# Optimization experiments

Hardware: AMD Instinct MI355X
Metric: run time of the kernel (lower is better)

Reference implementation:

```python
import jax, jax.numpy as jnp
import numpy as np
import math

B, S, D, H = 2, 2048, 1024, 16
DK = D // H


def setup_inputs() -> dict:
    key = jax.random.key(0)
    ks = jax.random.split(key, 12)
    scale = 1.0 / math.sqrt(D)
    inp = {
        "q": jax.random.normal(ks[0], (B, S, D), jnp.float32),
        "k": jax.random.normal(ks[1], (B, S, D), jnp.float32),
        "v": jax.random.normal(ks[2], (B, S, D), jnp.float32),
        # causal mask, broadcast over batch and heads; 0 entries are masked out
        "mask": jnp.tril(jnp.ones((S, S), jnp.int32))[None, None, :, :],
        "wq_w": jax.random.normal(ks[3], (D, D), jnp.float32) * scale,
        "wq_b": jax.random.normal(ks[4], (D,), jnp.float32) * 0.01,
        "wk_w": jax.random.normal(ks[5], (D, D), jnp.float32) * scale,
        "wk_b": jax.random.normal(ks[6], (D,), jnp.float32) * 0.01,
        "wv_w": jax.random.normal(ks[7], (D, D), jnp.float32) * scale,
        "wv_b": jax.random.normal(ks[8], (D,), jnp.float32) * 0.01,
        "wo_w": jax.random.normal(ks[9], (D, D), jnp.float32) * scale,
        "wo_b": jax.random.normal(ks[10], (D,), jnp.float32) * 0.01,
    }
    return inp


def _mha(q, k, v, mask, wq_w, wq_b, wk_w, wk_b, wv_w, wv_b, wo_w, wo_b):
    # nn.Linear: x @ W^T + b
    def split_heads(x):  # [B,S,D] -> [B,H,S,DK]
        return x.reshape(B, S, H, DK).transpose(0, 2, 1, 3)

    Q = split_heads(q @ wq_w.T + wq_b)
    K = split_heads(k @ wk_w.T + wk_b)
    V = split_heads(v @ wv_w.T + wv_b)

    scores = jnp.einsum("bhqd,bhkd->bhqk", Q, K) / math.sqrt(DK)  # [B,H,S,S]
    scores = jnp.where(mask == 0, jnp.float32(-1e9), scores)
    # NOTE: source uses softmax(dim=1) == over the HEADS axis; replicated faithfully.
    attn = jax.nn.softmax(scores, axis=1)
    out = jnp.einsum("bhqk,bhkd->bhqd", attn, V)  # [B,H,S,DK]
    out = out.transpose(0, 2, 1, 3).reshape(B, S, D)
    return out @ wo_w.T + wo_b


def reference(q, k, v, mask, wq_w, wq_b, wk_w, wk_b, wv_w, wv_b, wo_w, wo_b):
    return _mha(q, k, v, mask, wq_w, wq_b, wk_w, wk_b, wv_w, wv_b, wo_w, wo_b)
```

## Files before the change

kernel.cpp:

```cpp
#include <hip/hip_runtime.h>
#include <stdint.h>


#define BB 2
#define SS 2048
#define DD 1024
#define HH 16
#define DKK 64

typedef _Float16 f16;
typedef __attribute__((ext_vector_type(2))) _Float16 f16x2;
typedef __attribute__((ext_vector_type(8))) _Float16 f16x8;
typedef __attribute__((ext_vector_type(2))) __fp16 fp16x2_raw;
typedef __attribute__((ext_vector_type(4))) float f32x4;

typedef __attribute__((address_space(3))) uint32_t lds32_t;
typedef __attribute__((address_space(1))) uint32_t g32_t;

__device__ __forceinline__ void async_cp16(void* lds, const void* g){
    __builtin_amdgcn_global_load_lds((const g32_t*)g, (lds32_t*)lds, 16, 0, 0);
}

union U32H { uint32_t u; f16x2 h; fp16x2_raw hr; };

__device__ __forceinline__ uint32_t pk2(float a, float b){
    U32H c; c.hr = __builtin_amdgcn_cvt_pkrtz(a, b); return c.u;
}
__device__ __forceinline__ float h_lo(uint32_t w){ U32H c; c.u = w; return (float)c.h[0]; }
__device__ __forceinline__ float h_hi(uint32_t w){ U32H c; c.u = w; return (float)c.h[1]; }
__device__ __forceinline__ uint32_t pkmul(uint32_t a, uint32_t b){
    U32H x, y, r; x.u = a; y.u = b; r.h = x.h * y.h; return r.u;
}
__device__ __forceinline__ uint32_t pkadd(uint32_t a, uint32_t b){
    U32H x, y, r; x.u = a; y.u = b; r.h = x.h + y.h; return r.u;
}
__device__ __forceinline__ uint16_t f2h(float f){
    union { f16 h; uint16_t u; } c; c.h = (f16)f; return c.u;
}

__global__ __launch_bounds__(256) void cvt_all(
    const float* __restrict__ w0, const float* __restrict__ w1,
    const float* __restrict__ w2, const float* __restrict__ w3,
    const float* __restrict__ a0, const float* __restrict__ a1,
    const float* __restrict__ a2,
    uint16_t* __restrict__ dw0, uint16_t* __restrict__ dw1,
    uint16_t* __restrict__ dw2, uint16_t* __restrict__ dw3,
    uint16_t* __restrict__ da0, uint16_t* __restrict__ da1,
    uint16_t* __restrict__ da2)
{
    const int y = blockIdx.y;
    const float* s; uint16_t* d; int n4;
    switch (y) {
        case 0: s = w0; d = dw0; n4 = 262144; break;
        case 1: s = w1; d = dw1; n4 = 262144; break;
        case 2: s = w2; d = dw2; n4 = 262144; break;
        case 3: s = w3; d = dw3; n4 = 262144; break;
        case 4: s = a0; d = da0; n4 = 1048576; break;
        case 5: s = a1; d = da1; n4 = 1048576; break;
        default: s = a2; d = da2; n4 = 1048576; break;
    }
    int i = blockIdx.x * 256 + threadIdx.x;
    if (i >= n4) return;
    float4 v = ((const float4*)s)[i];
    ((uint2*)d)[i] = make_uint2(pk2(v.x, v.y), pk2(v.z, v.w));
}

template <int OMODE>
__device__ __forceinline__ void gemm_core(
    uint16_t (*As)[32], uint16_t (*Bs)[32],
    const uint16_t* __restrict__ A, const uint16_t* __restrict__ W,
    const float* __restrict__ bias, void* __restrict__ Cout,
    const int kbeg, const int kend)
{
    const int t    = threadIdx.x;
    const int bm   = blockIdx.x * 128;
    const int bn   = blockIdx.y * 128;
    const int lane = t & 63;
    const int w    = t >> 6;
    const int wm   = (w >> 1) * 64;
    const int wn   = (w & 1) * 64;
    const int lm   = lane & 15;
    const int quad = lane >> 4;

    f32x4 acc[4][4] = {};

    const int lr = lane >> 2;
    const int lc = (lane & 3) * 8;

    for (int k0 = kbeg; k0 < kend; k0 += 32) {
#pragma unroll
        for (int i2 = 0; i2 < 2; ++i2) {
            const int i = w * 2 + i2;
            async_cp16(&As[16*i][0], &A[(size_t)(bm + 16*i + lr) * DD + k0 + lc]);
            async_cp16(&Bs[16*i][0], &W[(size_t)(bn + 16*i + lr) * DD + k0 + lc]);
        }
        __syncthreads();
        f16x8 a8[4], b8[4];
#pragma unroll
        for (int mt = 0; mt < 4; ++mt) a8[mt] = *(const f16x8*)&As[wm + 16*mt + lm][quad*8];
#pragma unroll
        for (int nt = 0; nt < 4; ++nt) b8[nt] = *(const f16x8*)&Bs[wn + 16*nt + lm][quad*8];
#pragma unroll
        for (int mt = 0; mt < 4; ++mt)
#pragma unroll
            for (int nt = 0; nt < 4; ++nt)
                acc[mt][nt] = __builtin_amdgcn_mfma_f32_16x16x32_f16(a8[mt], b8[nt], acc[mt][nt], 0, 0, 0);
        __syncthreads();
    }

#pragma unroll
    for (int nt = 0; nt < 4; ++nt) {
        const int ng = bn + wn + 16*nt + lm;
        const float bv = bias ? bias[ng] : 0.0f;
#pragma unroll
        for (int mt = 0; mt < 4; ++mt) {
            const int m0 = bm + wm + 16*mt + quad*4;
            if (OMODE == 1) {
                const int bb = m0 >> 11, s0 = m0 & (SS - 1);
                const int hh = ng >> 6,  dk = ng & 63;
                uint2 wv;
                wv.x = pk2(acc[mt][nt][0] + bv, acc[mt][nt][1] + bv);
                wv.y = pk2(acc[mt][nt][2] + bv, acc[mt][nt][3] + bv);
                *(uint2*)&((uint16_t*)Cout)[(((size_t)(bb*HH + hh))*DKK + dk)*SS + s0] = wv;
            } else {
#pragma unroll
                for (int r = 0; r < 4; ++r) {
                    const int m = m0 + r;
                    const float val = acc[mt][nt][r] + bv;
                    if (OMODE == 0) {
                        const int bb = m >> 11, s = m & (SS - 1);
                        const int hh = ng >> 6, dk = ng & 63;
                        ((uint16_t*)Cout)[(((size_t)(bb*HH + hh))*SS + s)*DKK + dk] = f2h(val);
                    } else {
                        ((float*)Cout)[(size_t)m * DD + ng] = val;
                    }
                }
            }
        }
    }
}

__global__ __launch_bounds__(256) void gemm_qkv(
    const uint16_t* __restrict__ xq, const uint16_t* __restrict__ wq,
    const float* __restrict__ bq, uint16_t* __restrict__ Qc,
    const uint16_t* __restrict__ xk, const uint16_t* __restrict__ wk,
    const float* __restrict__ bk, uint16_t* __restrict__ Kc,
    const uint16_t* __restrict__ xv, const uint16_t* __restrict__ wv,
    const float* __restrict__ bv, uint16_t* __restrict__ Vt)
{
    __shared__ __align__(16) uint16_t As[128][32];
    __shared__ __align__(16) uint16_t Bs[128][32];
    const int z = blockIdx.z;
    if (z == 0)      gemm_core<0>(As, Bs, xq, wq, bq, Qc, 0, DD);
    else if (z == 1) gemm_core<0>(As, Bs, xk, wk, bk, Kc, 0, DD);
    else             gemm_core<1>(As, Bs, xv, wv, bv, Vt, 0, DD);
}

__global__ __launch_bounds__(256) void gemm_o_split(
    const uint16_t* __restrict__ A, const uint16_t* __restrict__ W,
    const float* __restrict__ bias, float* __restrict__ P0, float* __restrict__ P1)
{
    __shared__ __align__(16) uint16_t As[128][32];
    __shared__ __align__(16) uint16_t Bs[128][32];
    const int z = blockIdx.z;
    if (z == 0) gemm_core<2>(As, Bs, A, W, bias,    (void*)P0, 0,   512);
    else        gemm_core<2>(As, Bs, A, W, nullptr, (void*)P1, 512, 1024);
}

__global__ __launch_bounds__(256) void addf4(
    const float* __restrict__ a, const float* __restrict__ b, float* __restrict__ o)
{
    const int i = blockIdx.x * 256 + threadIdx.x;
    float4 x = ((const float4*)a)[i];
    float4 y = ((const float4*)b)[i];
    ((float4*)o)[i] = make_float4(x.x+y.x, x.y+y.y, x.z+y.z, x.w+y.w);
}

__global__ __launch_bounds__(256) void suf_kernel(
    const uint16_t* __restrict__ Vt, float* __restrict__ Suf)
{
    const int bh = blockIdx.x;
    const int t  = threadIdx.x;
    const int d = t & 63, seg = t >> 6;
    __shared__ float cs[64][65];
    const uint16_t* row = Vt + ((size_t)bh * DKK + d) * SS;
    for (int cl = 0; cl < 16; ++cl) {
        const int c = seg * 16 + cl;
        float sum = 0.f;
#pragma unroll
        for (int jj = 0; jj < 4; ++jj) {
            uint4 u = *(const uint4*)&row[c * 32 + jj * 8];
            sum += ((h_lo(u.x)+h_hi(u.x)) + (h_lo(u.y)+h_hi(u.y)))
                 + ((h_lo(u.z)+h_hi(u.z)) + (h_lo(u.w)+h_hi(u.w)));
        }
        cs[c][d] = sum;
    }
    __syncthreads();
    if (t < 64) {
        float run = 0.f;
        Suf[((size_t)bh * 65 + 64) * DKK + t] = 0.f;
        for (int c = 63; c >= 0; --c) {
            run += cs[c][t];
            Suf[((size_t)bh * 65 + c) * DKK + t] = run;
        }
    }
}

__global__ __launch_bounds__(1024, 4) void attn_v11(
    const uint16_t* __restrict__ Qc, const uint16_t* __restrict__ Kc,
    const uint16_t* __restrict__ Vt, const float* __restrict__ Suf,
    uint16_t* __restrict__ AOp)
{
    __shared__ __align__(16) uint16_t E[3][16][32][40];
    __shared__ __align__(16) uint16_t Zr[2][32][40];

    const int x  = blockIdx.x;
    const int p  = x & 3;
    const int b  = (x >> 2) & 1;
    const int pr = x >> 3;
    const int tid  = threadIdx.x;
    const int h    = tid >> 6;
    const int lane = tid & 63;
    const int lm   = lane & 15;
    const int quad = lane >> 4;

    const uint16_t* Qh = Qc + ((size_t)(b*HH + h)) * SS * DKK;
    const uint16_t* Kh = Kc + ((size_t)(b*HH + h)) * SS * DKK;
    const uint16_t* Vh = Vt + ((size_t)(b*HH + h)) * DKK * SS;
    uint16_t* AOb = AOp + ((size_t)(p*BB + b)) * SS * DD;

    const int rq  = tid >> 4;
    const int rk2 = tid & 15;

#pragma unroll
    for (int tt = 0; tt < 2; ++tt) {
        const int tq = tt ? (63 - pr) : pr;
        const int q0 = tq * 32;
        const int nch = (tq >= p) ? ((tq - p) >> 2) + 1 : 0;

        f16x8 qf[2][2];
#pragma unroll
        for (int qt = 0; qt < 2; ++qt)
#pragma unroll
            for (int kd = 0; kd < 2; ++kd)
                qf[qt][kd] = *(const f16x8*)&Qh[(size_t)(q0 + 16*qt + lm)*DKK + kd*32 + quad*8];

        f32x4 oacc[2][4] = {};

        auto LOADK = [&](int c, f16x8* kf) {
            const int k0 = c * 32;
#pragma unroll
            for (int kt = 0; kt < 2; ++kt) {
                kf[2*kt+0] = *(const f16x8*)&Kh[(size_t)(k0 + 16*kt + lm)*DKK + quad*8];
                kf[2*kt+1] = *(const f16x8*)&Kh[(size_t)(k0 + 16*kt + lm)*DKK + 32 + quad*8];
            }
        };
        auto LOADV = [&](int c, f16x8* vf) {
            const int k0 = c * 32;
#pragma unroll
            for (int dt = 0; dt < 4; ++dt)
                vf[dt] = *(const f16x8*)&Vh[(size_t)(16*dt + lm)*SS + k0 + quad*8];
        };

        auto SCORES_C = [&](int c, int ebw, const f16x8* kf) {
            const int k0 = c * 32;
            f32x4 sacc[2][2] = {};
#pragma unroll
            for (int kt = 0; kt < 2; ++kt)
#pragma unroll
                for (int qt = 0; qt < 2; ++qt) {
                    sacc[kt][qt] = __builtin_amdgcn_mfma_f32_16x16x32_f16(kf[2*kt+0], qf[qt][0], sacc[kt][qt], 0, 0, 0);
                    sacc[kt][qt] = __builtin_amdgcn_mfma_f32_16x16x32_f16(kf[2*kt+1], qf[qt][1], sacc[kt][qt], 0, 0, 0);
                }
#pragma unroll
            for (int kt = 0; kt < 2; ++kt)
#pragma unroll
                for (int qt = 0; qt < 2; ++qt) {
                    const int kh = k0 + 16*kt, qh = q0 + 16*qt;
                    uint2 evw;
                    if (kh + 15 <= qh) {
                        evw.x = pk2(__expf(sacc[kt][qt][0] * 0.125f), __expf(sacc[kt][qt][1] * 0.125f));
                        evw.y = pk2(__expf(sacc[kt][qt][2] * 0.125f), __expf(sacc[kt][qt][3] * 0.125f));
                    } else if (kh > qh + 15) {
                        evw.x = 0x3C003C00u; evw.y = 0x3C003C00u;
                    } else {
                        const int qg = qh + lm;
                        float e[4];
#pragma unroll
                        for (int r = 0; r < 4; ++r) {
                            const int kg = kh + quad*4 + r;
                            e[r] = (kg > qg) ? 1.0f : __expf(sacc[kt][qt][r] * 0.125f);
                        }
                        evw = make_uint2(pk2(e[0], e[1]), pk2(e[2], e[3]));
                    }
                    *(uint2*)&E[ebw][h][16*qt + lm][16*kt + quad*4] = evw;
                }
        };

        auto HEADSUM = [&](int ebr, int zbw) {
            uint32_t t8[8];
#pragma unroll
            for (int i = 0; i < 8; ++i)
                t8[i] = pkadd(*(const uint32_t*)&E[ebr][i][rq][rk2*2],
                              *(const uint32_t*)&E[ebr][i+8][rq][rk2*2]);
            uint32_t s0 = pkadd(pkadd(t8[0], t8[4]), pkadd(t8[1], t8[5]));
            uint32_t s1 = pkadd(pkadd(t8[2], t8[6]), pkadd(t8[3], t8[7]));
            uint32_t s  = pkadd(s0, s1);
            *(uint32_t*)&Zr[zbw][rq][rk2*2] =
                pk2(__fdividef(1.f, h_lo(s)), __fdividef(1.f, h_hi(s)));
        };

        auto PV = [&](int ebr, int zbr, const f16x8* vf) {
#pragma unroll
            for (int qt = 0; qt < 2; ++qt) {
                uint4 eu = *(const uint4*)&E[ebr][h][16*qt + lm][quad*8];
                uint4 zu = *(const uint4*)&Zr[zbr][16*qt + lm][quad*8];
                union { uint4 u; f16x8 v; } P;
                P.u.x = pkmul(eu.x, zu.x); P.u.y = pkmul(eu.y, zu.y);
                P.u.z = pkmul(eu.z, zu.z); P.u.w = pkmul(eu.w, zu.w);
#pragma unroll
                for (int dt = 0; dt < 4; ++dt)
                    oacc[qt][dt] = __builtin_amdgcn_mfma_f32_16x16x32_f16(P.v, vf[dt], oacc[qt][dt], 0, 0, 0);
            }
        };

        __syncthreads();

        if (nch > 0) {
            {
                f16x8 kf[4];
                LOADK(p, kf);
                SCORES_C(p, 0, kf);
            }
            __syncthreads();
            int eb = 0;
            for (int n = 0; n < nch; ++n) {
                const int c  = p + 4*n;
                const int zb = n & 1;
                f16x8 vf[4], kf[4];
                if (n > 0)       LOADV(c - 4, vf);
                if (n + 1 < nch) LOADK(c + 4, kf);
                if (tid < 512)   HEADSUM(eb, zb);
                if (n + 1 < nch) SCORES_C(c + 4, (eb + 1) % 3, kf);
                if (n > 0)       PV((eb + 2) % 3, zb ^ 1, vf);
                __syncthreads();
                eb = (eb + 1 == 3) ? 0 : eb + 1;
            }
            {
                f16x8 vf[4];
                LOADV(p + 4*(nch - 1), vf);
                PV((eb + 2) % 3, (nch - 1) & 1, vf);
            }
        }

        float corr[4] = {0.f, 0.f, 0.f, 0.f};
        if (p == 0) {
            const float* Sf = Suf + ((size_t)(b*HH + h) * 65 + (tq + 1)) * DKK;
#pragma unroll
            for (int dt = 0; dt < 4; ++dt) corr[dt] = 0.0625f * Sf[16*dt + lm];
        }
#pragma unroll
        for (int qt = 0; qt < 2; ++qt)
#pragma unroll
            for (int dt = 0; dt < 4; ++dt)
#pragma unroll
                for (int r = 0; r < 4; ++r) {
                    const int s = q0 + 16*qt + quad*4 + r;
                    AOb[(size_t)s * DD + h*DKK + 16*dt + lm] = f2h(oacc[qt][dt][r] + corr[dt]);
                }
    }
}

__global__ __launch_bounds__(256) void reduce4(uint16_t* AOp)
{
    const size_t P1 = (size_t)BB * SS * DD;
    const int i = blockIdx.x * 256 + threadIdx.x;
    uint2 u0 = ((const uint2*)AOp)[i];
    uint2 u1 = ((const uint2*)(AOp + P1))[i];
    uint2 u2 = ((const uint2*)(AOp + 2*P1))[i];
    uint2 u3 = ((const uint2*)(AOp + 3*P1))[i];
    float r0 = (h_lo(u0.x) + h_lo(u1.x)) + (h_lo(u2.x) + h_lo(u3.x));
    float r1 = (h_hi(u0.x) + h_hi(u1.x)) + (h_hi(u2.x) + h_hi(u3.x));
    float r2 = (h_lo(u0.y) + h_lo(u1.y)) + (h_lo(u2.y) + h_lo(u3.y));
    float r3 = (h_hi(u0.y) + h_hi(u1.y)) + (h_hi(u2.y) + h_hi(u3.y));
    ((uint2*)AOp)[i] = make_uint2(pk2(r0, r1), pk2(r2, r3));
}

extern "C" void kernel_launch(void* const* d_in, const int* in_sizes, int n_in,
                              void* d_out, int out_size, void* d_ws, size_t ws_size,
                              hipStream_t stream)
{
    const float* q    = (const float*)d_in[0];
    const float* k    = (const float*)d_in[1];
    const float* v    = (const float*)d_in[2];
    const float* wq_w = (const float*)d_in[4];
    const float* wq_b = (const float*)d_in[5];
    const float* wk_w = (const float*)d_in[6];
    const float* wk_b = (const float*)d_in[7];
    const float* wv_w = (const float*)d_in[8];
    const float* wv_b = (const float*)d_in[9];
    const float* wo_w = (const float*)d_in[10];
    const float* wo_b = (const float*)d_in[11];
    float* out = (float*)d_out;

    uint16_t* wsu = (uint16_t*)d_ws;
    const size_t M1 = (size_t)1 << 20;
    uint16_t* wcq = wsu + 0 * M1;
    uint16_t* wck = wsu + 1 * M1;
    uint16_t* wcv = wsu + 2 * M1;
    uint16_t* wco = wsu + 3 * M1;
    uint16_t* Qc  = wsu + 4 * M1;
    uint16_t* Kc  = wsu + 8 * M1;
    uint16_t* Vt  = wsu + 12 * M1;
    uint16_t* AOp = wsu + 16 * M1;
    uint16_t* xq  = wsu + 16 * M1;
    uint16_t* xk  = wsu + 20 * M1;
    uint16_t* xv  = wsu + 24 * M1;
    float*    Suf = (float*)wcq;
    float*    P0  = (float*)(wsu + 20 * M1);
    float*    P1  = (float*)(wsu + 8 * M1);

    cvt_all<<<dim3(4096, 7), 256, 0, stream>>>(
        wq_w, wk_w, wv_w, wo_w, q, k, v,
        wcq, wck, wcv, wco, xq, xk, xv);

    gemm_qkv<<<dim3(32, 8, 3), 256, 0, stream>>>(
        xq, wcq, wq_b, Qc,
        xk, wck, wk_b, Kc,
        xv, wcv, wv_b, Vt);

    suf_kernel<<<32, 256, 0, stream>>>(Vt, Suf);
    attn_v11<<<256, 1024, 0, stream>>>(Qc, Kc, Vt, Suf, AOp);

    reduce4<<<4096, 256, 0, stream>>>(AOp);
    gemm_o_split<<<dim3(32, 8, 2), 256, 0, stream>>>(AOp, wco, wo_b, P0, P1);
    addf4<<<4096, 256, 0, stream>>>(P0, P1, out);
}
```

Baseline: 292.4 us.

## Restructure attention kernel to one 64-row query tile per block without pipelining

Each attention block now owns a single 64-row query tile instead of two balanced 32-row tiles. Every loaded K and V chunk is therefore reused across more query rows, and the triple-buffered exp storage and double-buffered reciprocal storage are replaced by single buffers behind three barriers per chunk. The change also switches the occupancy hint to a waves-per-EU attribute. It gives up the balanced pairing of short and long causal tiles and the overlap of head-sum, score and PV stages, so the blocks handling late query tiles carry much more work than the rest.

```diff
diff --git a/kernel.cpp b/kernel.cpp
--- a/kernel.cpp
+++ b/kernel.cpp
@@ -206,18 +206,19 @@
     }
 }
 
-__global__ __launch_bounds__(1024, 4) void attn_v11(
+__global__ __launch_bounds__(1024) __attribute__((amdgpu_waves_per_eu(4, 4)))
+void attn_v13(
     const uint16_t* __restrict__ Qc, const uint16_t* __restrict__ Kc,
     const uint16_t* __restrict__ Vt, const float* __restrict__ Suf,
     uint16_t* __restrict__ AOp)
 {
-    __shared__ __align__(16) uint16_t E[3][16][32][40];
-    __shared__ __align__(16) uint16_t Zr[2][32][40];
+    __shared__ __align__(16) uint16_t E[16][64][36];
+    __shared__ __align__(16) uint16_t Zr[64][36];
 
     const int x  = blockIdx.x;
     const int p  = x & 3;
     const int b  = (x >> 2) & 1;
-    const int pr = x >> 3;
+    const int t  = x >> 3;
     const int tid  = threadIdx.x;
     const int h    = tid >> 6;
     const int lane = tid & 63;
@@ -229,146 +230,109 @@
     const uint16_t* Vh = Vt + ((size_t)(b*HH + h)) * DKK * SS;
     uint16_t* AOb = AOp + ((size_t)(p*BB + b)) * SS * DD;
 
-    const int rq  = tid >> 4;
-    const int rk2 = tid & 15;
-
-#pragma unroll
-    for (int tt = 0; tt < 2; ++tt) {
-        const int tq = tt ? (63 - pr) : pr;
-        const int q0 = tq * 32;
-        const int nch = (tq >= p) ? ((tq - p) >> 2) + 1 : 0;
-
-        f16x8 qf[2][2];
-#pragma unroll
-        for (int qt = 0; qt < 2; ++qt)
-#pragma unroll
-            for (int kd = 0; kd < 2; ++kd)
-                qf[qt][kd] = *(const f16x8*)&Qh[(size_t)(q0 + 16*qt + lm)*DKK + kd*32 + quad*8];
-
-        f32x4 oacc[2][4] = {};
-
-        auto LOADK = [&](int c, f16x8* kf) {
-            const int k0 = c * 32;
-#pragma unroll
-            for (int kt = 0; kt < 2; ++kt) {
-                kf[2*kt+0] = *(const f16x8*)&Kh[(size_t)(k0 + 16*kt + lm)*DKK + quad*8];
-                kf[2*kt+1] = *(const f16x8*)&Kh[(size_t)(k0 + 16*kt + lm)*DKK + 32 + quad*8];
+    const int rq = tid >> 4;
+    const int uu = tid & 15;
+
+    const int q0   = t * 64;
+    const int cmax = 2*t + 1;
+    const int nch  = (cmax >= p) ? ((cmax - p) >> 2) + 1 : 0;
+
+    f16x8 qf[4][2];
+#pragma unroll
+    for (int qt = 0; qt < 4; ++qt)
+#pragma unroll
+        for (int kd = 0; kd < 2; ++kd)
+            qf[qt][kd] = *(const f16x8*)&Qh[(size_t)(q0 + 16*qt + lm)*DKK + kd*32 + quad*8];
+
+    f32x4 oacc[4][4] = {};
+
+    for (int n = 0; n < nch; ++n) {
+        const int c  = p + 4*n;
+        const int k0 = c * 32;
+        __syncthreads();
+#pragma unroll
+        for (int kt = 0; kt < 2; ++kt) {
+            f16x8 kf0 = *(const f16x8*)&Kh[(size_t)(k0 + 16*kt + lm)*DKK + quad*8];
+            f16x8 kf1 = *(const f16x8*)&Kh[(size_t)(k0 + 16*kt + lm)*DKK + 32 + quad*8];
+            f32x4 sacc[4] = {};
+#pragma unroll
+            for (int qt = 0; qt < 4; ++qt) {
+                sacc[qt] = __builtin_amdgcn_mfma_f32_16x16x32_f16(kf0, qf[qt][0], sacc[qt], 0, 0, 0);
+                sacc[qt] = __builtin_amdgcn_mfma_f32_16x16x32_f16(kf1, qf[qt][1], sacc[qt], 0, 0, 0);
             }
-        };
-        auto LOADV = [&](int c, f16x8* vf) {
-            const int k0 = c * 32;
-#pragma unroll
-            for (int dt = 0; dt < 4; ++dt)
-                vf[dt] = *(const f16x8*)&Vh[(size_t)(16*dt + lm)*SS + k0 + quad*8];
-        };
-
-        auto SCORES_C = [&](int c, int ebw, const f16x8* kf) {
-            const int k0 = c * 32;
-            f32x4 sacc[2][2] = {};
-#pragma unroll
-            for (int kt = 0; kt < 2; ++kt)
-#pragma unroll
-                for (int qt = 0; qt < 2; ++qt) {
-                    sacc[kt][qt] = __builtin_amdgcn_mfma_f32_16x16x32_f16(kf[2*kt+0], qf[qt][0], sacc[kt][qt], 0, 0, 0);
-                    sacc[kt][qt] = __builtin_amdgcn_mfma_f32_16x16x32_f16(kf[2*kt+1], qf[qt][1], sacc[kt][qt], 0, 0, 0);
+            const int kh = k0 + 16*kt;
+#pragma unroll
+            for (int qt = 0; qt < 4; ++qt) {
+                const int qh = q0 + 16*qt;
+                uint2 evw;
+                if (kh + 15 <= qh) {
+                    evw.x = pk2(__expf(sacc[qt][0] * 0.125f), __expf(sacc[qt][1] * 0.125f));
+                    evw.y = pk2(__expf(sacc[qt][2] * 0.125f), __expf(sacc[qt][3] * 0.125f));
+                } else if (kh > qh + 15) {
+                    evw.x = 0x3C003C00u; evw.y = 0x3C003C00u;
+                } else {
+                    const int qg = qh + lm;
+                    float e[4];
+#pragma unroll
+                    for (int r = 0; r < 4; ++r) {
+                        const int kg = kh + quad*4 + r;
+                        e[r] = (kg > qg) ? 1.0f : __expf(sacc[qt][r] * 0.125f);
+                    }
+                    evw = make_uint2(pk2(e[0], e[1]), pk2(e[2], e[3]));
                 }
-#pragma unroll
-            for (int kt = 0; kt < 2; ++kt)
-#pragma unroll
-                for (int qt = 0; qt < 2; ++qt) {
-                    const int kh = k0 + 16*kt, qh = q0 + 16*qt;
-                    uint2 evw;
-                    if (kh + 15 <= qh) {
-                        evw.x = pk2(__expf(sacc[kt][qt][0] * 0.125f), __expf(sacc[kt][qt][1] * 0.125f));
-                        evw.y = pk2(__expf(sacc[kt][qt][2] * 0.125f), __expf(sacc[kt][qt][3] * 0.125f));
-                    } else if (kh > qh + 15) {
-                        evw.x = 0x3C003C00u; evw.y = 0x3C003C00u;
-                    } else {
-                        const int qg = qh + lm;
-                        float e[4];
-#pragma unroll
-                        for (int r = 0; r < 4; ++r) {
-                            const int kg = kh + quad*4 + r;
-                            e[r] = (kg > qg) ? 1.0f : __expf(sacc[kt][qt][r] * 0.125f);
-                        }
-                        evw = make_uint2(pk2(e[0], e[1]), pk2(e[2], e[3]));
-                    }
-                    *(uint2*)&E[ebw][h][16*qt + lm][16*kt + quad*4] = evw;
-                }
-        };
-
-        auto HEADSUM = [&](int ebr, int zbw) {
+                *(uint2*)&E[h][16*qt + lm][16*kt + quad*4] = evw;
+            }
+        }
+        __syncthreads();
+        {
             uint32_t t8[8];
 #pragma unroll
             for (int i = 0; i < 8; ++i)
-                t8[i] = pkadd(*(const uint32_t*)&E[ebr][i][rq][rk2*2],
-                              *(const uint32_t*)&E[ebr][i+8][rq][rk2*2]);
+                t8[i] = pkadd(*(const uint32_t*)&E[i][rq][uu*2],
+                              *(const uint32_t*)&E[i+8][rq][uu*2]);
             uint32_t s0 = pkadd(pkadd(t8[0], t8[4]), pkadd(t8[1], t8[5]));
             uint32_t s1 = pkadd(pkadd(t8[2], t8[6]), pkadd(t8[3], t8[7]));
             uint32_t s  = pkadd(s0, s1);
-            *(uint32_t*)&Zr[zbw][rq][rk2*2] =
+            *(uint32_t*)&Zr[rq][uu*2] =
                 pk2(__fdividef(1.f, h_lo(s)), __fdividef(1.f, h_hi(s)));
-        };
-
-        auto PV = [&](int ebr, int zbr, const f16x8* vf) {
-#pragma unroll
-            for (int qt = 0; qt < 2; ++qt) {
-                uint4 eu = *(const uint4*)&E[ebr][h][16*qt + lm][quad*8];
-                uint4 zu = *(const uint4*)&Zr[zbr][16*qt + lm][quad*8];
-                union { uint4 u; f16x8 v; } P;
-                P.u.x = pkmul(eu.x, zu.x); P.u.y = pkmul(eu.y, zu.y);
-                P.u.z = pkmul(eu.z, zu.z); P.u.w = pkmul(eu.w, zu.w);
+        }
+        __syncthreads();
+        {
+            f16x8 vf[4];
+#pragma unroll
+            for (int dt = 0; dt < 4; ++dt)
+                vf[dt] = *(const f16x8*)&Vh[(size_t)(16*dt + lm)*SS + k0 + quad*8];
+#pragma unroll
+            for (int qt = 0; qt < 4; ++qt) {
+                uint2 e0 = *(const uint2*)&E[h][16*qt + lm][quad*8];
+                uint2 e1 = *(const uint2*)&E[h][16*qt + lm][quad*8 + 4];
+                uint2 z0 = *(const uint2*)&Zr[16*qt + lm][quad*8];
+                uint2 z1 = *(const uint2*)&Zr[16*qt + lm][quad*8 + 4];
+                union { uint32_t u[4]; f16x8 v; } P;
+                P.u[0] = pkmul(e0.x, z0.x); P.u[1] = pkmul(e0.y, z0.y);
+                P.u[2] = pkmul(e1.x, z1.x); P.u[3] = pkmul(e1.y, z1.y);
 #pragma unroll
                 for (int dt = 0; dt < 4; ++dt)
                     oacc[qt][dt] = __builtin_amdgcn_mfma_f32_16x16x32_f16(P.v, vf[dt], oacc[qt][dt], 0, 0, 0);
             }
-        };
-
-        __syncthreads();
-
-        if (nch > 0) {
-            {
-                f16x8 kf[4];
-                LOADK(p, kf);
-                SCORES_C(p, 0, kf);
+        }
+    }
+
+    float corr[4] = {0.f, 0.f, 0.f, 0.f};
+    if (p == 0) {
+        const float* Sf = Suf + ((size_t)(b*HH + h) * 65 + (cmax + 1)) * DKK;
+#pragma unroll
+        for (int dt = 0; dt < 4; ++dt) corr[dt] = 0.0625f * Sf[16*dt + lm];
+    }
+#pragma unroll
+    for (int qt = 0; qt < 4; ++qt)
+#pragma unroll
+        for (int dt = 0; dt < 4; ++dt)
+#pragma unroll
+            for (int r = 0; r < 4; ++r) {
+                const int s = q0 + 16*qt + quad*4 + r;
+                AOb[(size_t)s * DD + h*DKK + 16*dt + lm] = f2h(oacc[qt][dt][r] + corr[dt]);
             }
-            __syncthreads();
-            int eb = 0;
-            for (int n = 0; n < nch; ++n) {
-                const int c  = p + 4*n;
-                const int zb = n & 1;
-                f16x8 vf[4], kf[4];
-                if (n > 0)       LOADV(c - 4, vf);
-                if (n + 1 < nch) LOADK(c + 4, kf);
-                if (tid < 512)   HEADSUM(eb, zb);
-                if (n + 1 < nch) SCORES_C(c + 4, (eb + 1) % 3, kf);
-                if (n > 0)       PV((eb + 2) % 3, zb ^ 1, vf);
-                __syncthreads();
-                eb = (eb + 1 == 3) ? 0 : eb + 1;
-            }
-            {
-                f16x8 vf[4];
-                LOADV(p + 4*(nch - 1), vf);
-                PV((eb + 2) % 3, (nch - 1) & 1, vf);
-            }
-        }
-
-        float corr[4] = {0.f, 0.f, 0.f, 0.f};
-        if (p == 0) {
-            const float* Sf = Suf + ((size_t)(b*HH + h) * 65 + (tq + 1)) * DKK;
-#pragma unroll
-            for (int dt = 0; dt < 4; ++dt) corr[dt] = 0.0625f * Sf[16*dt + lm];
-        }
-#pragma unroll
-        for (int qt = 0; qt < 2; ++qt)
-#pragma unroll
-            for (int dt = 0; dt < 4; ++dt)
-#pragma unroll
-                for (int r = 0; r < 4; ++r) {
-                    const int s = q0 + 16*qt + quad*4 + r;
-                    AOb[(size_t)s * DD + h*DKK + 16*dt + lm] = f2h(oacc[qt][dt][r] + corr[dt]);
-                }
-    }
 }
 
 __global__ __launch_bounds__(256) void reduce4(uint16_t* AOp)
@@ -430,7 +394,7 @@
         xv, wcv, wv_b, Vt);
 
     suf_kernel<<<32, 256, 0, stream>>>(Vt, Suf);
-    attn_v11<<<256, 1024, 0, stream>>>(Qc, Kc, Vt, Suf, AOp);
+    attn_v13<<<256, 1024, 0, stream>>>(Qc, Kc, Vt, Suf, AOp);
 
     reduce4<<<4096, 256, 0, stream>>>(AOp);
     gemm_o_split<<<dim3(32, 8, 2), 256, 0, stream>>>(AOp, wco, wo_b, P0, P1);
```

Measured after the change: 340.0 us. +16.3%, slower.
